# Optimization experiments

Hardware: AMD Instinct MI355X
Metric: run time of the kernel (lower is better)

The kernel has to match this reference:

```python
import jax, jax.numpy as jnp
import numpy as np
from jax import lax

T, X, H = 16384, 512, 1024
A_SCALE, A_IDENTITY = 0.1, 0.9


def setup_inputs() -> dict:
    key = jax.random.key(0)
    k1, k2, k3 = jax.random.split(key, 3)
    x_seq = jax.random.normal(k1, (T, X), dtype=jnp.float32)
    h0 = jnp.zeros((H,), dtype=jnp.float32)
    # A_raw is orthogonal-initialized in the module; a random normal matrix
    # is fine as a correctness baseline (orthogonalize for numerical parity).
    A_raw = jax.random.normal(k2, (H, H), dtype=jnp.float32)
    A_raw, _ = jnp.linalg.qr(A_raw)
    B = jax.random.normal(k3, (H, X), dtype=jnp.float32) * (1.0 / np.sqrt(X))  # lecun_normal
    c = jnp.zeros((H,), dtype=jnp.float32)
    return {"x_seq": x_seq, "h0": h0, "A_raw": A_raw, "B": B, "c": c}


def reference(x_seq, h0, A_raw, B, c):
    # A = a_identity * I + a_scale * A_raw
    A = A_IDENTITY * jnp.eye(H, dtype=A_raw.dtype) + A_SCALE * A_raw
    # Precompute input projections for all timesteps in one GEMM: [T, H]
    Bx = x_seq @ B.T + c

    def step(h, bx_t):
        h_new = jnp.tanh(A @ h + bx_t)
        return h_new, h_new

    _, h_all = lax.scan(step, h0, Bx)
    return h_all
```

## Files before the change

### kernel.cpp

```cpp
#include <hip/hip_runtime.h>
#include <math.h>


#define T_STEPS 16384
#define XD 512
#define HD 1024

typedef unsigned int uint32x4 __attribute__((ext_vector_type(4)));

__global__ __launch_bounds__(256) void gemm_bx_kernel(
    const float* __restrict__ x, const float* __restrict__ B,
    const float* __restrict__ c, float* __restrict__ out)
{
    __shared__ __align__(16) float xs[32][68];
    __shared__ __align__(16) float bs[32][68];

    const int tid = threadIdx.x;
    const int t0 = blockIdx.x * 64;
    const int i0 = blockIdx.y * 64;
    const int tx = tid & 15;
    const int ty = tid >> 4;
    const int lr = tid >> 3;
    const int lc = (tid & 7) << 2;

    float acc[4][4] = {{0.f}};

    for (int k0 = 0; k0 < XD; k0 += 32) {
        const float4 xa = *(const float4*)&x[(size_t)(t0 + lr) * XD + k0 + lc];
        const float4 xb = *(const float4*)&x[(size_t)(t0 + lr + 32) * XD + k0 + lc];
        const float4 ba = *(const float4*)&B[(size_t)(i0 + lr) * XD + k0 + lc];
        const float4 bb = *(const float4*)&B[(size_t)(i0 + lr + 32) * XD + k0 + lc];
        __syncthreads();
        xs[lc + 0][lr] = xa.x; xs[lc + 1][lr] = xa.y; xs[lc + 2][lr] = xa.z; xs[lc + 3][lr] = xa.w;
        xs[lc + 0][lr + 32] = xb.x; xs[lc + 1][lr + 32] = xb.y; xs[lc + 2][lr + 32] = xb.z; xs[lc + 3][lr + 32] = xb.w;
        bs[lc + 0][lr] = ba.x; bs[lc + 1][lr] = ba.y; bs[lc + 2][lr] = ba.z; bs[lc + 3][lr] = ba.w;
        bs[lc + 0][lr + 32] = bb.x; bs[lc + 1][lr + 32] = bb.y; bs[lc + 2][lr + 32] = bb.z; bs[lc + 3][lr + 32] = bb.w;
        __syncthreads();
        #pragma unroll
        for (int k = 0; k < 32; ++k) {
            const float4 av = *(const float4*)&xs[k][ty << 2];
            const float4 bv = *(const float4*)&bs[k][tx << 2];
            const float am[4] = {av.x, av.y, av.z, av.w};
            const float bn[4] = {bv.x, bv.y, bv.z, bv.w};
            #pragma unroll
            for (int m = 0; m < 4; ++m)
                #pragma unroll
                for (int n = 0; n < 4; ++n)
                    acc[m][n] = fmaf(am[m], bn[n], acc[m][n]);
        }
    }

    #pragma unroll
    for (int m = 0; m < 4; ++m) {
        const int trow = t0 + (ty << 2) + m;
        #pragma unroll
        for (int n = 0; n < 4; ++n) {
            const int icol = i0 + (tx << 2) + n;
            out[(size_t)trow * HD + icol] = acc[m][n] + c[icol];
        }
    }
}

__global__ void init_slots_kernel(unsigned long long* slots, const float* h0)
{
    const int i = threadIdx.x;
    union { float f; unsigned u; } v; v.f = h0[i];
    slots[3 * HD + i] = (unsigned long long)v.u;
    slots[0 * HD + i] = 0xFFFFFFFF00000000ull;
    slots[1 * HD + i] = 0xFFFFFFFF00000000ull;
    slots[2 * HD + i] = 0xFFFFFFFF00000000ull;
}

__global__ __launch_bounds__(512) void rnn_scan_kernel(
    const float* __restrict__ A_raw, float* out,
    unsigned long long* slots)
{
    const int tid = threadIdx.x;
    const int bid = blockIdx.x;
    const int wave = tid >> 6;
    const int lane = tid & 63;
    const int r0 = (bid << 4) + (wave << 1);

    __shared__ float hlds[2][HD];

    float aw0[16], aw1[16];
    #pragma unroll
    for (int j = 0; j < 16; ++j) {
        const int k = lane + (j << 6);
        float v0 = 0.1f * A_raw[(size_t)r0 * HD + k];
        float v1 = 0.1f * A_raw[(size_t)(r0 + 1) * HD + k];
        if (k == r0) v0 += 0.9f;
        if (k == r0 + 1) v1 += 0.9f;
        aw0[j] = v0; aw1[j] = v1;
    }

    float2 bxn = *(const float2*)&out[r0];

    for (int t = 0; t < T_STEPS; ++t) {
        const float2 bx = bxn;

        const unsigned long long* sp =
            slots + ((size_t)((t + 3) & 3) << 10) + (tid << 1);
        uint32x4 s;
        do {
            asm volatile(
                "global_load_dwordx4 %0, %1, off sc0 sc1\n\t"
                "s_waitcnt vmcnt(0)"
                : "=v"(s) : "v"(sp));
        } while (s.y != (unsigned)t || s.w != (unsigned)t);

        union { unsigned u; float f; } c0, c1; c0.u = s.x; c1.u = s.z;
        *(float2*)&hlds[t & 1][tid << 1] = make_float2(c0.f, c1.f);
        __syncthreads();

        const int tn = (t + 1 < T_STEPS) ? (t + 1) : t;
        bxn = *(const float2*)&out[(size_t)tn * HD + r0];

        const float* hl = hlds[t & 1];
        float p0 = 0.f, p1 = 0.f;
        #pragma unroll
        for (int j = 0; j < 16; ++j) {
            const float hvj = hl[lane + (j << 6)];
            p0 = fmaf(aw0[j], hvj, p0);
            p1 = fmaf(aw1[j], hvj, p1);
        }

        #pragma unroll
        for (int off = 32; off >= 1; off >>= 1) {
            p0 += __shfl_xor(p0, off, 64);
            p1 += __shfl_xor(p1, off, 64);
        }

        if (lane == 0) {
            const float h0n = tanhf(p0 + bx.x);
            const float h1n = tanhf(p1 + bx.y);
            *(float2*)&out[(size_t)t * HD + r0] = make_float2(h0n, h1n);
            union { float f; unsigned u; } u0, u1; u0.f = h0n; u1.f = h1n;
            uint32x4 pkt;
            pkt.x = u0.u; pkt.y = (unsigned)(t + 1);
            pkt.z = u1.u; pkt.w = (unsigned)(t + 1);
            unsigned long long* dp = slots + ((size_t)(t & 3) << 10) + r0;
            asm volatile(
                "global_store_dwordx4 %0, %1, off sc0 sc1"
                :: "v"(dp), "v"(pkt) : "memory");
        }
    }
}

extern "C" void kernel_launch(void* const* d_in, const int* in_sizes, int n_in,
                              void* d_out, int out_size, void* d_ws, size_t ws_size,
                              hipStream_t stream)
{
    const float* x     = (const float*)d_in[0];
    const float* h0    = (const float*)d_in[1];
    const float* A_raw = (const float*)d_in[2];
    const float* B     = (const float*)d_in[3];
    const float* c     = (const float*)d_in[4];
    float* out = (float*)d_out;
    unsigned long long* slots = (unsigned long long*)d_ws;

    dim3 gemm_grid(T_STEPS / 64, HD / 64);
    gemm_bx_kernel<<<gemm_grid, 256, 0, stream>>>(x, B, c, out);
    init_slots_kernel<<<1, HD, 0, stream>>>(slots, h0);
    rnn_scan_kernel<<<64, 512, 0, stream>>>(A_raw, out, slots);
}
```

Measured before the change: 24.45 ms.

## Pin scan blocks to a single XCD and poll slots with cheaper loads

The scan kernel now launches 512 blocks. Each block reads its XCC_ID and counts arrivals per XCD through atomics, and the first XCD to collect 64 blocks claims the work. The other blocks exit, so all 64 working blocks share one XCD's L2 and the per-step handoff of h does not have to cross dies. Polling first uses loads with only sc0 (L2-coherent) and falls back to system-scope sc0 sc1 loads after a few spins. The slot ring shrinks from 4 to 3 buffers. This adds an election prologue and extra blocks that exit immediately, and it relies on the cross-CU visibility semantics of sc0 loads and on 64 co-resident blocks fitting on one XCD.

```diff
diff --git a/kernel.cpp b/kernel.cpp
--- a/kernel.cpp
+++ b/kernel.cpp
@@ -61,22 +61,47 @@
     }
 }
 
-__global__ void init_slots_kernel(unsigned long long* slots, const float* h0)
+__global__ void init_slots_kernel(unsigned long long* slots, unsigned* ctrl,
+                                  const float* h0)
 {
     const int i = threadIdx.x;
     union { float f; unsigned u; } v; v.f = h0[i];
-    slots[3 * HD + i] = (unsigned long long)v.u;
+    slots[2 * HD + i] = (unsigned long long)v.u;
     slots[0 * HD + i] = 0xFFFFFFFF00000000ull;
     slots[1 * HD + i] = 0xFFFFFFFF00000000ull;
-    slots[2 * HD + i] = 0xFFFFFFFF00000000ull;
-}
-
-__global__ __launch_bounds__(512) void rnn_scan_kernel(
+    if (i < 9) ctrl[i] = (i == 8) ? 0xFFFFFFFFu : 0u;
+}
+
+__global__ __launch_bounds__(512, 4) void rnn_scan_kernel(
     const float* __restrict__ A_raw, float* out,
-    unsigned long long* slots)
-{
+    unsigned long long* slots, unsigned* ctrl)
+{
+    __shared__ int s_bid;
+    if (threadIdx.x == 0) {
+        unsigned xcd;
+        asm volatile("s_getreg_b32 %0, hwreg(HW_REG_XCC_ID)" : "=s"(xcd));
+        xcd &= 7u;
+        int my = -1;
+        const unsigned slot = atomicAdd(&ctrl[xcd], 1u);
+        if (slot < 64u) {
+            if (slot == 63u) atomicCAS(&ctrl[8], 0xFFFFFFFFu, xcd);
+            unsigned w;
+            const unsigned* wp = &ctrl[8];
+            do {
+                asm volatile(
+                    "global_load_dword %0, %1, off sc0 sc1\n\t"
+                    "s_waitcnt vmcnt(0)"
+                    : "=v"(w) : "v"(wp));
+            } while (w == 0xFFFFFFFFu);
+            if (w == xcd) my = (int)slot;
+        }
+        s_bid = my;
+    }
+    __syncthreads();
+    const int bid = s_bid;
+    if (bid < 0) return;
+
     const int tid = threadIdx.x;
-    const int bid = blockIdx.x;
     const int wave = tid >> 6;
     const int lane = tid & 63;
     const int r0 = (bid << 4) + (wave << 1);
@@ -96,18 +121,31 @@
 
     float2 bxn = *(const float2*)&out[r0];
 
+    int cs = 2;
+    int ps = 0;
+
     for (int t = 0; t < T_STEPS; ++t) {
         const float2 bx = bxn;
 
         const unsigned long long* sp =
-            slots + ((size_t)((t + 3) & 3) << 10) + (tid << 1);
+            slots + ((size_t)cs << 10) + (tid << 1);
         uint32x4 s;
-        do {
-            asm volatile(
-                "global_load_dwordx4 %0, %1, off sc0 sc1\n\t"
-                "s_waitcnt vmcnt(0)"
-                : "=v"(s) : "v"(sp));
-        } while (s.y != (unsigned)t || s.w != (unsigned)t);
+        int spin = 0;
+        for (;;) {
+            if (__builtin_expect(spin < 6, 1)) {
+                asm volatile(
+                    "global_load_dwordx4 %0, %1, off sc0\n\t"
+                    "s_waitcnt vmcnt(0)"
+                    : "=v"(s) : "v"(sp));
+            } else {
+                asm volatile(
+                    "global_load_dwordx4 %0, %1, off sc0 sc1\n\t"
+                    "s_waitcnt vmcnt(0)"
+                    : "=v"(s) : "v"(sp));
+            }
+            if (s.y == (unsigned)t && s.w == (unsigned)t) break;
+            ++spin;
+        }
 
         union { unsigned u; float f; } c0, c1; c0.u = s.x; c1.u = s.z;
         *(float2*)&hlds[t & 1][tid << 1] = make_float2(c0.f, c1.f);
@@ -139,11 +177,13 @@
             uint32x4 pkt;
             pkt.x = u0.u; pkt.y = (unsigned)(t + 1);
             pkt.z = u1.u; pkt.w = (unsigned)(t + 1);
-            unsigned long long* dp = slots + ((size_t)(t & 3) << 10) + r0;
+            unsigned long long* dp = slots + ((size_t)ps << 10) + r0;
             asm volatile(
                 "global_store_dwordx4 %0, %1, off sc0 sc1"
                 :: "v"(dp), "v"(pkt) : "memory");
         }
+        cs = ps;
+        ps = (ps + 1 == 3) ? 0 : ps + 1;
     }
 }
 
@@ -158,9 +198,10 @@
     const float* c     = (const float*)d_in[4];
     float* out = (float*)d_out;
     unsigned long long* slots = (unsigned long long*)d_ws;
+    unsigned* ctrl = (unsigned*)(slots + 3 * HD);
 
     dim3 gemm_grid(T_STEPS / 64, HD / 64);
     gemm_bx_kernel<<<gemm_grid, 256, 0, stream>>>(x, B, c, out);
-    init_slots_kernel<<<1, HD, 0, stream>>>(slots, h0);
-    rnn_scan_kernel<<<64, 512, 0, stream>>>(A_raw, out, slots);
-}
+    init_slots_kernel<<<1, HD, 0, stream>>>(slots, ctrl, h0);
+    rnn_scan_kernel<<<512, 512, 0, stream>>>(A_raw, out, slots, ctrl);
+}
```

New measurement: 58.18 ms. +137.9%, slower.
